# Kernel optimization log

Measured on AMD Instinct MI355X. Metric: run time of the kernel, lower is better.

The kernel has to match this reference:

```python
import jax, jax.numpy as jnp
import numpy as np

INPUT_SIZE, HIDDEN_SIZE, OUTPUT_SIZE = 63, 32, 1

def setup_inputs() -> dict:
    key = jax.random.key(0)
    ks = jax.random.split(key, 12)
    stdv = 1.0 / np.sqrt(HIDDEN_SIZE)
    u = lambda k, shape: jax.random.uniform(k, shape, jnp.float32, -stdv, stdv)
    return {
        "input": jax.random.normal(ks[0], (4096, 512, INPUT_SIZE), jnp.float32),
        "w_xz": u(ks[1], (INPUT_SIZE, HIDDEN_SIZE)),
        "w_hz": u(ks[2], (HIDDEN_SIZE, HIDDEN_SIZE)),
        "b_z": u(ks[3], (HIDDEN_SIZE,)),
        "w_xr": u(ks[4], (INPUT_SIZE, HIDDEN_SIZE)),
        "w_hr": u(ks[5], (HIDDEN_SIZE, HIDDEN_SIZE)),
        "b_r": u(ks[6], (HIDDEN_SIZE,)),
        "w_xh": u(ks[7], (INPUT_SIZE, HIDDEN_SIZE)),
        "w_hh": u(ks[8], (HIDDEN_SIZE, HIDDEN_SIZE)),
        "b_h": u(ks[9], (HIDDEN_SIZE,)),
        "w_out": u(ks[10], (HIDDEN_SIZE, OUTPUT_SIZE)),
        "b_out": u(ks[11], (OUTPUT_SIZE,)),
    }

def reference(input, w_xz, w_hz, b_z, w_xr, w_hr, b_r, w_xh, w_hh, b_h, w_out, b_out):
    B = input.shape[0]
    # precompute input projections for all steps in 3 batched GEMMs: [B,T,H]
    xz = jnp.einsum("bti,ih->bth", input, w_xz) + b_z
    xr = jnp.einsum("bti,ih->bth", input, w_xr) + b_r
    xh = jnp.einsum("bti,ih->bth", input, w_xh) + b_h

    def step(h, xs):
        xz_t, xr_t, xh_t = xs
        z = jax.nn.sigmoid(xz_t + h @ w_hz)
        r = jax.nn.sigmoid(xr_t + h @ w_hr)
        h_tilde = jnp.tanh(xh_t + (r * h) @ w_hh)
        h = (1.0 - z) * h + z * h_tilde
        return h, None

    h0 = jnp.zeros((B, HIDDEN_SIZE), input.dtype)
    # scan over time axis (move T to leading)
    xs = (jnp.swapaxes(xz, 0, 1), jnp.swapaxes(xr, 0, 1), jnp.swapaxes(xh, 0, 1))
    h_last, _ = jax.lax.scan(step, h0, xs)
    return jax.nn.sigmoid(h_last @ w_out + b_out)
```

## Files before the change

kernel.cpp:

```cpp
#include <hip/hip_runtime.h>

#define BATCH 4096
#define T 512
#define ISZ 63
#define H 32
#define CT 8

__global__ __launch_bounds__(192, 3) void gru_fused(
    const float* __restrict__ x,
    const float* __restrict__ w_xz, const float* __restrict__ w_hz, const float* __restrict__ b_z,
    const float* __restrict__ w_xr, const float* __restrict__ w_hr, const float* __restrict__ b_r,
    const float* __restrict__ w_xh, const float* __restrict__ w_hh, const float* __restrict__ b_h,
    const float* __restrict__ w_out, const float* __restrict__ b_out,
    float* __restrict__ out)
{
    __shared__ __align__(16) float x_lds[2][CT][64];
    __shared__ __align__(16) float h_lds[2][H];
    __shared__ __align__(16) float z_lds[2][H];
    __shared__ __align__(16) float rh_lds[2][H];

    const int tid  = threadIdx.x;
    const int wav  = tid >> 6;
    const int bsub = (tid >> 5) & 1;
    const int j    = tid & 31;

    const float* wxp = (wav == 0) ? w_xz : (wav == 1) ? w_xr : w_xh;
    const float* whp = (wav == 0) ? w_hz : (wav == 1) ? w_hr : w_hh;
    const float* bp  = (wav == 0) ? b_z  : (wav == 1) ? b_r  : b_h;

    float wx[ISZ];
    float wh[H];
    #pragma unroll
    for (int i = 0; i < ISZ; ++i) wx[i] = wxp[i * H + j];
    #pragma unroll
    for (int k = 0; k < H; ++k)  wh[k] = whp[k * H + j];
    const float bias = bp[j];

    for (int pair = 0; pair < 2; ++pair) {
        const int b0 = blockIdx.x * 4 + pair * 2;

        if (tid < 64) h_lds[tid >> 5][tid & 31] = 0.f;
        __syncthreads();

        for (int c = 0; c < T / CT; ++c) {
            const size_t gbase = ((size_t)b0 * T + (size_t)c * CT) * ISZ;
            for (int idx = tid; idx < 2 * CT * ISZ; idx += 192) {
                int bb = idx / (CT * ISZ);
                int f  = idx - bb * (CT * ISZ);
                int tt = f / ISZ;
                int ii = f - tt * ISZ;
                x_lds[bb][tt][ii] = x[gbase + (size_t)bb * (T * ISZ) + f];
            }
            __syncthreads();

            for (int tt = 0; tt < CT; ++tt) {
                float acc = bias;
                const float4* xr4 = (const float4*)(&x_lds[bsub][tt][0]);
                #pragma unroll
                for (int i4 = 0; i4 < 15; ++i4) {
                    float4 v = xr4[i4];
                    acc = fmaf(v.x, wx[4*i4+0], acc);
                    acc = fmaf(v.y, wx[4*i4+1], acc);
                    acc = fmaf(v.z, wx[4*i4+2], acc);
                    acc = fmaf(v.w, wx[4*i4+3], acc);
                }
                acc = fmaf(x_lds[bsub][tt][60], wx[60], acc);
                acc = fmaf(x_lds[bsub][tt][61], wx[61], acc);
                acc = fmaf(x_lds[bsub][tt][62], wx[62], acc);

                if (wav < 2) {
                    const float4* hr4 = (const float4*)(&h_lds[bsub][0]);
                    #pragma unroll
                    for (int k4 = 0; k4 < 8; ++k4) {
                        float4 v = hr4[k4];
                        acc = fmaf(v.x, wh[4*k4+0], acc);
                        acc = fmaf(v.y, wh[4*k4+1], acc);
                        acc = fmaf(v.z, wh[4*k4+2], acc);
                        acc = fmaf(v.w, wh[4*k4+3], acc);
                    }
                    float s = __fdividef(1.f, 1.f + __expf(-acc));
                    if (wav == 0) z_lds[bsub][j] = s;
                    else          rh_lds[bsub][j] = s * h_lds[bsub][j];
                }
                __syncthreads();

                if (wav == 2) {
                    const float4* rr4 = (const float4*)(&rh_lds[bsub][0]);
                    #pragma unroll
                    for (int k4 = 0; k4 < 8; ++k4) {
                        float4 v = rr4[k4];
                        acc = fmaf(v.x, wh[4*k4+0], acc);
                        acc = fmaf(v.y, wh[4*k4+1], acc);
                        acc = fmaf(v.z, wh[4*k4+2], acc);
                        acc = fmaf(v.w, wh[4*k4+3], acc);
                    }
                    float e    = __expf(-2.f * acc);
                    float htld = __fdividef(1.f - e, 1.f + e);
                    float zval = z_lds[bsub][j];
                    float hold = h_lds[bsub][j];
                    h_lds[bsub][j] = fmaf(zval, htld - hold, hold);
                }
                __syncthreads();
            }
        }

        if (wav == 2) {
            float p = h_lds[bsub][j] * w_out[j];
            #pragma unroll
            for (int off = 16; off >= 1; off >>= 1) p += __shfl_xor(p, off);
            if (j == 0) out[b0 + bsub] = __fdividef(1.f, 1.f + __expf(-(p + b_out[0])));
        }
        __syncthreads();
    }
}

extern "C" void kernel_launch(void* const* d_in, const int* in_sizes, int n_in,
                              void* d_out, int out_size, void* d_ws, size_t ws_size,
                              hipStream_t stream) {
    const float* x     = (const float*)d_in[0];
    const float* w_xz  = (const float*)d_in[1];
    const float* w_hz  = (const float*)d_in[2];
    const float* b_z   = (const float*)d_in[3];
    const float* w_xr  = (const float*)d_in[4];
    const float* w_hr  = (const float*)d_in[5];
    const float* b_r   = (const float*)d_in[6];
    const float* w_xh  = (const float*)d_in[7];
    const float* w_hh  = (const float*)d_in[8];
    const float* b_h   = (const float*)d_in[9];
    const float* w_out = (const float*)d_in[10];
    const float* b_out = (const float*)d_in[11];
    float* out = (float*)d_out;

    dim3 grid(BATCH / 4), block(192);
    hipLaunchKernelGGL(gru_fused, grid, block, 0, stream,
                       x, w_xz, w_hz, b_z, w_xr, w_hr, b_r,
                       w_xh, w_hh, b_h, w_out, b_out, out);
}
```

Measured before the change: 2.382 ms.

## Software-pipeline input projection and split dot products into multiple accumulators

Computes the input projection for the next timestep while waiting between barriers, so only the short recurrent dot product sits on the serial critical path. Dot products now use four independent accumulators to break the FMA dependency chain. Empty asm constraints pin the weights in VGPRs. The prefetch costs extra registers under the existing launch bounds and reorders floating-point summation slightly.

```diff
diff --git a/kernel.cpp b/kernel.cpp
--- a/kernel.cpp
+++ b/kernel.cpp
@@ -34,7 +34,42 @@
     for (int i = 0; i < ISZ; ++i) wx[i] = wxp[i * H + j];
     #pragma unroll
     for (int k = 0; k < H; ++k)  wh[k] = whp[k * H + j];
-    const float bias = bp[j];
+    float bias = bp[j];
+    #pragma unroll
+    for (int i = 0; i < ISZ; ++i) asm volatile("" : "+v"(wx[i]));
+    #pragma unroll
+    for (int k = 0; k < H; ++k)  asm volatile("" : "+v"(wh[k]));
+
+    auto xdot = [&](int tt) -> float {
+        const float* xp = &x_lds[bsub][tt][0];
+        float a0 = 0.f, a1 = 0.f, a2 = 0.f, a3 = 0.f;
+        const float4* x4 = (const float4*)xp;
+        #pragma unroll
+        for (int i4 = 0; i4 < 15; ++i4) {
+            float4 v = x4[i4];
+            a0 = fmaf(v.x, wx[4*i4+0], a0);
+            a1 = fmaf(v.y, wx[4*i4+1], a1);
+            a2 = fmaf(v.z, wx[4*i4+2], a2);
+            a3 = fmaf(v.w, wx[4*i4+3], a3);
+        }
+        a0 = fmaf(xp[60], wx[60], a0);
+        a1 = fmaf(xp[61], wx[61], a1);
+        a2 = fmaf(xp[62], wx[62], a2);
+        return (a0 + a1) + (a2 + a3);
+    };
+    auto hdot = [&](const float* hp) -> float {
+        float a0 = 0.f, a1 = 0.f, a2 = 0.f, a3 = 0.f;
+        const float4* h4 = (const float4*)hp;
+        #pragma unroll
+        for (int k4 = 0; k4 < 8; ++k4) {
+            float4 v = h4[k4];
+            a0 = fmaf(v.x, wh[4*k4+0], a0);
+            a1 = fmaf(v.y, wh[4*k4+1], a1);
+            a2 = fmaf(v.z, wh[4*k4+2], a2);
+            a3 = fmaf(v.w, wh[4*k4+3], a3);
+        }
+        return (a0 + a1) + (a2 + a3);
+    };
 
     for (int pair = 0; pair < 2; ++pair) {
         const int b0 = blockIdx.x * 4 + pair * 2;
@@ -53,54 +88,31 @@
             }
             __syncthreads();
 
+            float xacc = xdot(0) + bias;
+
             for (int tt = 0; tt < CT; ++tt) {
-                float acc = bias;
-                const float4* xr4 = (const float4*)(&x_lds[bsub][tt][0]);
-                #pragma unroll
-                for (int i4 = 0; i4 < 15; ++i4) {
-                    float4 v = xr4[i4];
-                    acc = fmaf(v.x, wx[4*i4+0], acc);
-                    acc = fmaf(v.y, wx[4*i4+1], acc);
-                    acc = fmaf(v.z, wx[4*i4+2], acc);
-                    acc = fmaf(v.w, wx[4*i4+3], acc);
-                }
-                acc = fmaf(x_lds[bsub][tt][60], wx[60], acc);
-                acc = fmaf(x_lds[bsub][tt][61], wx[61], acc);
-                acc = fmaf(x_lds[bsub][tt][62], wx[62], acc);
-
+                float xnext = 0.f;
                 if (wav < 2) {
-                    const float4* hr4 = (const float4*)(&h_lds[bsub][0]);
-                    #pragma unroll
-                    for (int k4 = 0; k4 < 8; ++k4) {
-                        float4 v = hr4[k4];
-                        acc = fmaf(v.x, wh[4*k4+0], acc);
-                        acc = fmaf(v.y, wh[4*k4+1], acc);
-                        acc = fmaf(v.z, wh[4*k4+2], acc);
-                        acc = fmaf(v.w, wh[4*k4+3], acc);
-                    }
+                    float acc = xacc + hdot(&h_lds[bsub][0]);
                     float s = __fdividef(1.f, 1.f + __expf(-acc));
                     if (wav == 0) z_lds[bsub][j] = s;
                     else          rh_lds[bsub][j] = s * h_lds[bsub][j];
+                    if (tt < CT - 1) xnext = xdot(tt + 1) + bias;
+                } else {
+                    if (tt < CT - 1) xnext = xdot(tt + 1) + bias;
                 }
                 __syncthreads();
 
                 if (wav == 2) {
-                    const float4* rr4 = (const float4*)(&rh_lds[bsub][0]);
-                    #pragma unroll
-                    for (int k4 = 0; k4 < 8; ++k4) {
-                        float4 v = rr4[k4];
-                        acc = fmaf(v.x, wh[4*k4+0], acc);
-                        acc = fmaf(v.y, wh[4*k4+1], acc);
-                        acc = fmaf(v.z, wh[4*k4+2], acc);
-                        acc = fmaf(v.w, wh[4*k4+3], acc);
-                    }
+                    float acc = xacc + hdot(&rh_lds[bsub][0]);
                     float e    = __expf(-2.f * acc);
                     float htld = __fdividef(1.f - e, 1.f + e);
-                    float zval = z_lds[bsub][j];
+                    float zv   = z_lds[bsub][j];
                     float hold = h_lds[bsub][j];
-                    h_lds[bsub][j] = fmaf(zval, htld - hold, hold);
+                    h_lds[bsub][j] = fmaf(zv, htld - hold, hold);
                 }
                 __syncthreads();
+                xacc = xnext;
             }
         }
 
```

Result: slower. 4.611 ms (+93.6%).
